# Optimization experiments

Measured on AMD Instinct MI355X. Metric: run time of the kernel, lower is better.

The kernel has to match this reference:

```python
import jax, jax.numpy as jnp
import numpy as np

NUM_EXPERTS = 8
EMBED_DIM = 1024
BATCH, SEQ = 4, 2048


def setup_inputs() -> dict:
    key = jax.random.key(0)
    k1, k2, k3 = jax.random.split(key, 3)
    E_symb = jax.random.normal(k1, (BATCH, SEQ, EMBED_DIM), dtype=jnp.float32)
    gate_w = jax.random.normal(k2, (EMBED_DIM, NUM_EXPERTS), dtype=jnp.float32) * 0.02
    gate_b = jnp.zeros((NUM_EXPERTS,), dtype=jnp.float32)
    expert_w = jax.random.normal(k3, (NUM_EXPERTS, EMBED_DIM, EMBED_DIM), dtype=jnp.float32) * 0.02
    return {"E_symb": E_symb, "gate_w": gate_w, "gate_b": gate_b,
            "expert_w": expert_w, "k": 2}


def reference(E_symb, gate_w, gate_b, expert_w, k):
    B, S, D = E_symb.shape
    E = expert_w.shape[0]
    x = E_symb.reshape(-1, D)                       # [T, D]
    logits = x @ gate_w + gate_b                    # [T, E]
    probs = jax.nn.softmax(logits.astype(jnp.float32), axis=-1)
    # top-k selection; NOTE: original renormalizes routing_weights but never
    # applies them to expert outputs -> combine is an UNWEIGHTED sum.
    _, sel = jax.lax.top_k(probs, k)                # [T, k]
    mask = jax.nn.one_hot(sel, E, dtype=x.dtype).sum(axis=1)  # [T, E] in {0,1}
    # dense grouped-GEMM then masked combine (replaces per-expert gather/scatter loop)
    y = jnp.einsum('td,edf->tef', x, expert_w)      # [T, E, D]
    out = jnp.einsum('tef,te->tf', y, mask)         # [T, D]
    return out.reshape(B, S, D)
```

## Files before the change

### kernel.cpp

```cpp
#include <hip/hip_runtime.h>
#include <hip/hip_bf16.h>
#include <stdint.h>

#define T_TOK 8192
#define DIM   1024
#define NEXP  8
#define BM    128
#define BN    128
#define BK2   32
#define NR_ROUTE 256

typedef __bf16 bf16_t;
typedef bf16_t bf16x8 __attribute__((ext_vector_type(8)));
typedef bf16_t bf16x4 __attribute__((ext_vector_type(4)));
typedef bf16_t bf16x2 __attribute__((ext_vector_type(2)));
typedef float  f32x4  __attribute__((ext_vector_type(4)));

#define WS_CNT    0
#define CIDX(p)   ((p) << 4)
#define WS_LIST   8192
#define WS_XBF    (4u << 20)
#define WS_W2     (20u << 20)
#define WS_NEED_PSUM ((size_t)76 << 20)

__device__ const int d_PA[28] = {0,0,0,0,0,0,0,1,1,1,1,1,1,2,2,2,2,2,3,3,3,3,4,4,4,5,5,6};
__device__ const int d_PB[28] = {1,2,3,4,5,6,7,2,3,4,5,6,7,3,4,5,6,7,4,5,6,7,5,6,7,6,7,7};

__device__ __forceinline__ void gload16(const void* g, void* l) {
    __builtin_amdgcn_global_load_lds(
        (const __attribute__((address_space(1))) unsigned int*)g,
        (__attribute__((address_space(3))) unsigned int*)l, 16, 0, 0);
}

__device__ __forceinline__ int swz32(int r, int k) {
    return ((r * BK2 + k) * 2) ^ (((r >> 1) & 3) << 4);
}

#define WAITCNT_VM0()   do { asm volatile("s_waitcnt vmcnt(0)" ::: "memory"); \
                             __builtin_amdgcn_sched_barrier(0); } while (0)
#define WAITCNT_VM4()   do { asm volatile("s_waitcnt vmcnt(4)" ::: "memory"); \
                             __builtin_amdgcn_sched_barrier(0); } while (0)
#define WAITCNT_LGKM0() do { asm volatile("s_waitcnt lgkmcnt(0)" ::: "memory"); \
                             __builtin_amdgcn_sched_barrier(0); } while (0)
#define BARRIER()       do { __builtin_amdgcn_s_barrier(); \
                             __builtin_amdgcn_sched_barrier(0); } while (0)

__global__ void zero_cnt(int4* cnt4) {
    cnt4[threadIdx.x] = int4{0, 0, 0, 0};
}

template <int PSUM>
__global__ __launch_bounds__(256) void fused_pre(const float* __restrict__ x,
                                                 const float* __restrict__ gw,
                                                 const float* __restrict__ gb,
                                                 const float* __restrict__ ew,
                                                 bf16_t* __restrict__ xbf,
                                                 bf16_t* __restrict__ w2,
                                                 int* __restrict__ cnt,
                                                 int* __restrict__ list) {
    __shared__ __align__(16) float sh[NEXP * DIM];
    int bx  = blockIdx.x;
    int tid = threadIdx.x;
    if (bx < NR_ROUTE) {
        float4 gb0 = *(const float4*)gb;
        float4 gb1 = *(const float4*)(gb + 4);
        float gbl[8] = {gb0.x, gb0.y, gb0.z, gb0.w, gb1.x, gb1.y, gb1.z, gb1.w};
        float* gwt = sh;
        const float4* gw4 = (const float4*)gw;
        #pragma unroll
        for (int i = 0; i < 8; i++) {
            int f4 = tid + i * 256;
            float4 v = gw4[f4];
            int d  = f4 >> 1;
            int e0 = (f4 & 1) * 4;
            gwt[(e0 + 0) * DIM + d] = v.x;
            gwt[(e0 + 1) * DIM + d] = v.y;
            gwt[(e0 + 2) * DIM + d] = v.z;
            gwt[(e0 + 3) * DIM + d] = v.w;
        }
        __syncthreads();
        int wid  = tid >> 6;
        int lane = tid & 63;
        const float4* gwt4 = (const float4*)gwt;
        for (int tt = 0; tt < 8; tt++) {
            int t = bx * 32 + wid * 8 + tt;
            const float4* xr4 = (const float4*)(x + (size_t)t * DIM);
            float acc[NEXP] = {};
            #pragma unroll
            for (int j = 0; j < 4; j++) {
                int c4 = j * 64 + lane;
                float4 v = xr4[c4];
                bf16x4 b;
                b[0] = (bf16_t)v.x; b[1] = (bf16_t)v.y;
                b[2] = (bf16_t)v.z; b[3] = (bf16_t)v.w;
                *(bf16x4*)(xbf + (size_t)t * DIM + c4 * 4) = b;
                #pragma unroll
                for (int e = 0; e < NEXP; e++) {
                    float4 g = gwt4[e * 256 + c4];
                    acc[e] += v.x * g.x + v.y * g.y + v.z * g.z + v.w * g.w;
                }
            }
            for (int off = 32; off >= 1; off >>= 1)
                #pragma unroll
                for (int e = 0; e < NEXP; e++)
                    acc[e] += __shfl_xor(acc[e], off, 64);
            if (lane == 0) {
                float logit[NEXP];
                #pragma unroll
                for (int e = 0; e < NEXP; e++) logit[e] = acc[e] + gbl[e];
                int b1 = 0; float best = logit[0];
                for (int e = 1; e < NEXP; e++) if (logit[e] > best) { best = logit[e]; b1 = e; }
                int b2 = -1; float best2 = -3.0e38f;
                for (int e = 0; e < NEXP; e++) {
                    if (e == b1) continue;
                    if (logit[e] > best2) { best2 = logit[e]; b2 = e; }
                }
                int a = min(b1, b2), bb = max(b1, b2);
                int p = a * 8 + bb;
                int pos = atomicAdd(&cnt[CIDX(p)], 1);
                list[p * T_TOK + pos] = t;
            }
        }
    } else if (PSUM) {
        int bz = bx - NR_ROUTE;
        int f0 = (bz & 15) * 64;
        int d0 = (bz >> 4) * 32;
        typedef bf16_t (*TileT)[64][32];
        TileT T = (TileT)sh;
        int dp = (tid & 15) * 2;
        int f4 = tid >> 4;
        #pragma unroll
        for (int e = 0; e < 8; e++) {
            const float* b0 = ew + ((size_t)e * DIM + d0 + dp) * DIM + f0 + f4 * 4;
            float4 u0 = *(const float4*)b0;
            float4 u1 = *(const float4*)(b0 + DIM);
            float a0[4] = {u0.x, u0.y, u0.z, u0.w};
            float a1[4] = {u1.x, u1.y, u1.z, u1.w};
            #pragma unroll
            for (int j = 0; j < 4; j++) {
                bf16x2 w;
                w[0] = (bf16_t)a0[j];
                w[1] = (bf16_t)a1[j];
                *(bf16x2*)&T[e][f4 * 4 + j][dp] = w;
            }
        }
        __syncthreads();
        const int PA[28] = {0,0,0,0,0,0,0,1,1,1,1,1,1,2,2,2,2,2,3,3,3,3,4,4,4,5,5,6};
        const int PB[28] = {1,2,3,4,5,6,7,2,3,4,5,6,7,3,4,5,6,7,4,5,6,7,5,6,7,6,7,7};
        int f  = tid >> 2;
        int dd = (tid & 3) * 8;
        #pragma unroll
        for (int pk = 0; pk < 28; pk++) {
            bf16x8 u = *(const bf16x8*)&T[PA[pk]][f][dd];
            bf16x8 v = *(const bf16x8*)&T[PB[pk]][f][dd];
            bf16x8 o;
            #pragma unroll
            for (int i = 0; i < 8; i++) o[i] = (bf16_t)((float)u[i] + (float)v[i]);
            *(bf16x8*)(w2 + (size_t)pk * DIM * DIM + (size_t)(f0 + f) * DIM + d0 + dd) = o;
        }
    } else {
        int bz  = bx - NR_ROUTE;
        int g   = bz >> 8;
        int rem = bz & 255;
        int f0  = (rem & 15) * 64;
        int d0  = (rem >> 4) * 64;
        float (*tile)[65] = (float (*)[65])sh;
        const float* s1 = ew + ((size_t)g * DIM + d0) * DIM + f0;
        int fl = (tid & 15) * 4;
        int dl = tid >> 4;
        #pragma unroll
        for (int i = 0; i < 4; i++) {
            int d = dl + i * 16;
            float4 u = *(const float4*)(s1 + (size_t)d * DIM + fl);
            tile[d][fl + 0] = u.x; tile[d][fl + 1] = u.y;
            tile[d][fl + 2] = u.z; tile[d][fl + 3] = u.w;
        }
        __syncthreads();
        bf16_t* dst = w2 + ((size_t)g * DIM + f0) * DIM + d0;
        int dl2 = (tid & 7) * 8;
        int fl2 = tid >> 3;
        #pragma unroll
        for (int i = 0; i < 2; i++) {
            int f = fl2 + i * 32;
            bf16x8 o;
            #pragma unroll
            for (int c = 0; c < 8; c++) o[c] = (bf16_t)tile[dl2 + c][f];
            *(bf16x8*)(dst + (size_t)f * DIM + dl2) = o;
        }
    }
}

template <int PSUM>
__global__ __launch_bounds__(256, 4) void moe_gemm(const bf16_t* __restrict__ xbf,
                                                   const bf16_t* __restrict__ wsrc,
                                                   const int* __restrict__ cnt,
                                                   const int* __restrict__ list,
                                                   float* __restrict__ out) {
    __shared__ __align__(16) bf16_t As[2][BM * BK2];
    __shared__ __align__(16) bf16_t Bs[2][BN * BK2];
    __shared__ int toks[BM];
    __shared__ int s_desc[128];
    __shared__ int s_ntile;
    int tid  = threadIdx.x;
    int lane = tid & 63;
    int wv   = tid >> 6;
    int wm   = wv >> 1, wn = wv & 1;

    if (tid < 64) {
        int c  = cnt[CIDX(tid)];
        int tp = (c + BM - 1) >> 7;
        int pre = 0, tot = 0;
        for (int i = 0; i < 64; i++) {
            int v = __shfl(tp, i, 64);
            if (i < tid) pre += v;
            tot += v;
        }
        for (int j = 0; j < tp; j++)
            s_desc[pre + j] = tid | ((j * BM) << 8);
        if (tid == 0) s_ntile = tot;
    }
    __syncthreads();
    int nwork = s_ntile * (DIM / BN);
    int q = nwork >> 3, r = nwork & 7;
    int xcd  = blockIdx.x & 7;
    int slot = blockIdx.x >> 3;
    int share = q + (xcd < r ? 1 : 0);
    if (slot >= share) return;
    int w = xcd * q + min(xcd, r) + slot;

    int dsc = s_desc[w >> 3];
    int n0  = (w & 7) * BN;
    int p   = dsc & 63;
    int m0  = dsc >> 8;
    int e1  = p >> 3, e2 = p & 7;
    int cp  = cnt[CIDX(p)];
    int valid = min(BM, cp - m0);
    if (tid < BM) toks[tid] = list[p * T_TOK + m0 + min(tid, valid - 1)];
    __syncthreads();

    const bf16_t* asrc[2];
    #pragma unroll
    for (int i = 0; i < 2; i++) {
        int c = i * 256 + tid;
        int rr = c >> 2, js = (c & 3) ^ ((rr >> 1) & 3);
        asrc[i] = xbf + (size_t)toks[rr] * DIM + js * 8;
    }

    f32x4 acc[4][4] = {};
    int lr = lane & 15;
    int lk = (lane >> 4) * 8;

    if (PSUM) {
        const bf16_t* bsrc[2];
        int pk = e1 * 7 - (e1 * (e1 - 1)) / 2 + (e2 - e1 - 1);
        const bf16_t* bb = wsrc + (size_t)pk * DIM * DIM;
        #pragma unroll
        for (int i = 0; i < 2; i++) {
            int c = i * 256 + tid;
            int rr = c >> 2, js = (c & 3) ^ ((rr >> 1) & 3);
            bsrc[i] = bb + (size_t)(n0 + rr) * DIM + js * 8;
        }
        #pragma unroll
        for (int i = 0; i < 2; i++)
            gload16(asrc[i], &As[0][(i * 256 + wv * 64) * 8]);
        #pragma unroll
        for (int i = 0; i < 2; i++)
            gload16(bsrc[i], &Bs[0][(i * 256 + wv * 64) * 8]);

        for (int ks = 0; ks < DIM / BK2; ks++) {
            int cur = ks & 1;
            if (ks < DIM / BK2 - 1) {
                int k1 = (ks + 1) * BK2;
                #pragma unroll
                for (int i = 0; i < 2; i++)
                    gload16(asrc[i] + k1, &As[cur ^ 1][(i * 256 + wv * 64) * 8]);
                #pragma unroll
                for (int i = 0; i < 2; i++)
                    gload16(bsrc[i] + k1, &Bs[cur ^ 1][(i * 256 + wv * 64) * 8]);
                WAITCNT_VM4();
            } else {
                WAITCNT_VM0();
            }
            BARRIER();
            const char* Ab = (const char*)As[cur];
            const char* Bb = (const char*)Bs[cur];
            bf16x8 af[4], bfr[4];
            #pragma unroll
            for (int mf = 0; mf < 4; mf++)
                af[mf] = *(const bf16x8*)(Ab + swz32(wm * 64 + mf * 16 + lr, lk));
            #pragma unroll
            for (int nf = 0; nf < 4; nf++)
                bfr[nf] = *(const bf16x8*)(Bb + swz32(wn * 64 + nf * 16 + lr, lk));
            #pragma unroll
            for (int mf = 0; mf < 4; mf++)
                #pragma unroll
                for (int nf = 0; nf < 4; nf++)
                    acc[mf][nf] = __builtin_amdgcn_mfma_f32_16x16x32_bf16(
                        af[mf], bfr[nf], acc[mf][nf], 0, 0, 0);
            BARRIER();
        }
    } else {
        const bf16_t* wt1 = wsrc + (size_t)e1 * DIM * DIM;
        const bf16_t* wt2 = wsrc + (size_t)e2 * DIM * DIM;
        for (int ks = 0; ks < DIM / BK2; ks++) {
            int k0 = ks * BK2;
            #pragma unroll
            for (int i = 0; i < 2; i++)
                gload16(asrc[i] + k0, &As[0][(i * 256 + wv * 64) * 8]);
            #pragma unroll
            for (int i = 0; i < 2; i++) {
                int c = i * 256 + tid;
                int f = c >> 2, j = c & 3;
                const bf16_t* s1 = wt1 + (size_t)(n0 + f) * DIM + k0 + j * 8;
                const bf16_t* s2 = wt2 + (size_t)(n0 + f) * DIM + k0 + j * 8;
                bf16x8 u = *(const bf16x8*)s1, w2v = *(const bf16x8*)s2, o;
                #pragma unroll
                for (int t = 0; t < 8; t++) o[t] = (bf16_t)((float)u[t] + (float)w2v[t]);
                *(bf16x8*)((char*)Bs[0] + swz32(f, j * 8)) = o;
            }
            WAITCNT_LGKM0();
            WAITCNT_VM0();
            BARRIER();
            const char* Ab = (const char*)As[0];
            const char* Bb = (const char*)Bs[0];
            bf16x8 af[4], bfr[4];
            #pragma unroll
            for (int mf = 0; mf < 4; mf++)
                af[mf] = *(const bf16x8*)(Ab + swz32(wm * 64 + mf * 16 + lr, lk));
            #pragma unroll
            for (int nf = 0; nf < 4; nf++)
                bfr[nf] = *(const bf16x8*)(Bb + swz32(wn * 64 + nf * 16 + lr, lk));
            #pragma unroll
            for (int mf = 0; mf < 4; mf++)
                #pragma unroll
                for (int nf = 0; nf < 4; nf++)
                    acc[mf][nf] = __builtin_amdgcn_mfma_f32_16x16x32_bf16(
                        af[mf], bfr[nf], acc[mf][nf], 0, 0, 0);
            BARRIER();
        }
    }

    #pragma unroll
    for (int mf = 0; mf < 4; mf++) {
        #pragma unroll
        for (int reg = 0; reg < 4; reg++) {
            int rl = wm * 64 + mf * 16 + (lane >> 4) * 4 + reg;
            if (rl < valid) {
                size_t trow = (size_t)toks[rl] * DIM;
                #pragma unroll
                for (int nf = 0; nf < 4; nf++)
                    out[trow + n0 + wn * 64 + nf * 16 + lr] = acc[mf][nf][reg];
            }
        }
    }
}

extern "C" void kernel_launch(void* const* d_in, const int* in_sizes, int n_in,
                              void* d_out, int out_size, void* d_ws, size_t ws_size,
                              hipStream_t stream) {
    const float* x  = (const float*)d_in[0];
    const float* gw = (const float*)d_in[1];
    const float* gb = (const float*)d_in[2];
    const float* ew = (const float*)d_in[3];
    float* out = (float*)d_out;
    char* ws = (char*)d_ws;
    int*    cnt  = (int*)(ws + WS_CNT);
    int*    list = (int*)(ws + WS_LIST);
    bf16_t* xbf  = (bf16_t*)(ws + WS_XBF);
    bf16_t* w2   = (bf16_t*)(ws + WS_W2);
    bool psum = (ws_size >= WS_NEED_PSUM);

    zero_cnt<<<dim3(1), 256, 0, stream>>>((int4*)cnt);
    if (psum) {
        fused_pre<1><<<dim3(NR_ROUTE + 512), 256, 0, stream>>>(x, gw, gb, ew,
                                                               xbf, w2, cnt, list);
        moe_gemm<1><<<dim3(1024), 256, 0, stream>>>(xbf, w2, cnt, list, out);
    } else {
        fused_pre<0><<<dim3(NR_ROUTE + 8 * 256), 256, 0, stream>>>(x, gw, gb, ew,
                                                                   xbf, w2, cnt, list);
        moe_gemm<0><<<dim3(1024), 256, 0, stream>>>(xbf, w2, cnt, list, out);
    }
}
```

Measured before the change: 76.33 us.

## Split routing into more blocks and restage pair-sum transpose through padded LDS

Routing now uses four times as many blocks, each handling 8 tokens instead of 32, to spread the gating work across more CUs. The pair-sum weight path now stages each expert's fp32 tile in a padded LDS array, then transposes and converts it into a padded bf16 tile. This targets strided, bank-conflicting LDS writes. In exchange it adds two barriers per expert, and every routing block reloads the full gate weight matrix into LDS, so that redundant load traffic goes up.

```diff
diff --git a/kernel.cpp b/kernel.cpp
--- a/kernel.cpp
+++ b/kernel.cpp
@@ -8,12 +8,11 @@
 #define BM    128
 #define BN    128
 #define BK2   32
-#define NR_ROUTE 256
+#define NR_ROUTE 1024
 
 typedef __bf16 bf16_t;
 typedef bf16_t bf16x8 __attribute__((ext_vector_type(8)));
 typedef bf16_t bf16x4 __attribute__((ext_vector_type(4)));
-typedef bf16_t bf16x2 __attribute__((ext_vector_type(2)));
 typedef float  f32x4  __attribute__((ext_vector_type(4)));
 
 #define WS_CNT    0
@@ -58,14 +57,14 @@
                                                  bf16_t* __restrict__ w2,
                                                  int* __restrict__ cnt,
                                                  int* __restrict__ list) {
-    __shared__ __align__(16) float sh[NEXP * DIM];
+    __shared__ __align__(16) char sh[45184];
     int bx  = blockIdx.x;
     int tid = threadIdx.x;
     if (bx < NR_ROUTE) {
         float4 gb0 = *(const float4*)gb;
         float4 gb1 = *(const float4*)(gb + 4);
         float gbl[8] = {gb0.x, gb0.y, gb0.z, gb0.w, gb1.x, gb1.y, gb1.z, gb1.w};
-        float* gwt = sh;
+        float* gwt = (float*)sh;
         const float4* gw4 = (const float4*)gw;
         #pragma unroll
         for (int i = 0; i < 8; i++) {
@@ -82,8 +81,8 @@
         int wid  = tid >> 6;
         int lane = tid & 63;
         const float4* gwt4 = (const float4*)gwt;
-        for (int tt = 0; tt < 8; tt++) {
-            int t = bx * 32 + wid * 8 + tt;
+        for (int tt = 0; tt < 2; tt++) {
+            int t = bx * 8 + wid * 2 + tt;
             const float4* xr4 = (const float4*)(x + (size_t)t * DIM);
             float acc[NEXP] = {};
             #pragma unroll
@@ -125,38 +124,43 @@
         int bz = bx - NR_ROUTE;
         int f0 = (bz & 15) * 64;
         int d0 = (bz >> 4) * 32;
-        typedef bf16_t (*TileT)[64][32];
-        TileT T = (TileT)sh;
-        int dp = (tid & 15) * 2;
-        int f4 = tid >> 4;
-        #pragma unroll
+        float (*stg)[65] = (float (*)[65])sh;
+        bf16_t* T = (bf16_t*)(sh + 8320);
+        int fc = tid & 15, dr = tid >> 4;
+        int fr = tid >> 2, dc = tid & 3;
         for (int e = 0; e < 8; e++) {
-            const float* b0 = ew + ((size_t)e * DIM + d0 + dp) * DIM + f0 + f4 * 4;
-            float4 u0 = *(const float4*)b0;
-            float4 u1 = *(const float4*)(b0 + DIM);
-            float a0[4] = {u0.x, u0.y, u0.z, u0.w};
-            float a1[4] = {u1.x, u1.y, u1.z, u1.w};
-            #pragma unroll
-            for (int j = 0; j < 4; j++) {
-                bf16x2 w;
-                w[0] = (bf16_t)a0[j];
-                w[1] = (bf16_t)a1[j];
-                *(bf16x2*)&T[e][f4 * 4 + j][dp] = w;
-            }
-        }
-        __syncthreads();
-        const int PA[28] = {0,0,0,0,0,0,0,1,1,1,1,1,1,2,2,2,2,2,3,3,3,3,4,4,4,5,5,6};
-        const int PB[28] = {1,2,3,4,5,6,7,2,3,4,5,6,7,3,4,5,6,7,4,5,6,7,5,6,7,6,7,7};
-        int f  = tid >> 2;
-        int dd = (tid & 3) * 8;
+            #pragma unroll
+            for (int it = 0; it < 2; it++) {
+                int d = dr + it * 16;
+                float4 v = *(const float4*)(ew + ((size_t)e * DIM + d0 + d) * DIM
+                                            + f0 + fc * 4);
+                stg[d][fc * 4 + 0] = v.x; stg[d][fc * 4 + 1] = v.y;
+                stg[d][fc * 4 + 2] = v.z; stg[d][fc * 4 + 3] = v.w;
+            }
+            __syncthreads();
+            bf16x4 o0, o1;
+            #pragma unroll
+            for (int c = 0; c < 4; c++) o0[c] = (bf16_t)stg[dc * 8 + c][fr];
+            #pragma unroll
+            for (int c = 0; c < 4; c++) o1[c] = (bf16_t)stg[dc * 8 + 4 + c][fr];
+            *(bf16x4*)&T[(e * 64 + fr) * 36 + dc * 8]     = o0;
+            *(bf16x4*)&T[(e * 64 + fr) * 36 + dc * 8 + 4] = o1;
+            __syncthreads();
+        }
         #pragma unroll
         for (int pk = 0; pk < 28; pk++) {
-            bf16x8 u = *(const bf16x8*)&T[PA[pk]][f][dd];
-            bf16x8 v = *(const bf16x8*)&T[PB[pk]][f][dd];
+            const bf16_t* ta = &T[(d_PA[pk] * 64 + fr) * 36 + dc * 8];
+            const bf16_t* tb = &T[(d_PB[pk] * 64 + fr) * 36 + dc * 8];
+            bf16x4 a0 = *(const bf16x4*)ta, a1 = *(const bf16x4*)(ta + 4);
+            bf16x4 b0 = *(const bf16x4*)tb, b1 = *(const bf16x4*)(tb + 4);
             bf16x8 o;
             #pragma unroll
-            for (int i = 0; i < 8; i++) o[i] = (bf16_t)((float)u[i] + (float)v[i]);
-            *(bf16x8*)(w2 + (size_t)pk * DIM * DIM + (size_t)(f0 + f) * DIM + d0 + dd) = o;
+            for (int i = 0; i < 4; i++) {
+                o[i]     = (bf16_t)((float)a0[i] + (float)b0[i]);
+                o[4 + i] = (bf16_t)((float)a1[i] + (float)b1[i]);
+            }
+            *(bf16x8*)(w2 + (size_t)pk * DIM * DIM + (size_t)(f0 + fr) * DIM
+                       + d0 + dc * 8) = o;
         }
     } else {
         int bz  = bx - NR_ROUTE;
```

Measured after the change: 68.96 us, median of 2. 1.11x faster.
